# Kernel optimization log

Measured on AMD Instinct MI355X. Metric: run time of the kernel, lower is better.

## Reference

```python
import jax, jax.numpy as jnp
import numpy as np

# Clos factorization for in=out=4096, middle_switch_multiplier=4:
BIN, B1, B2, B3, BOUT = 64, 64, 256, 64, 64
B, C, D = 2, 4096, 4096


def setup_inputs() -> dict:
    key = jax.random.key(0)
    ks = jax.random.split(key, 7)
    k = 1.0 / np.sqrt(D)
    x = jax.random.normal(ks[0], (B, C, D), dtype=jnp.float32)
    # kaiming_uniform(a=sqrt(5)) on [bin,b1,b2]-like tensors ~ uniform(-bound, bound)
    w1 = jax.random.uniform(ks[1], (BIN, B1, B2), jnp.float32, -k, k)
    w2 = jax.random.uniform(ks[2], (B1, B2, B3), jnp.float32, -k, k)
    w3 = jax.random.uniform(ks[3], (B2, B3, BOUT), jnp.float32, -k, k)
    bias1 = jax.random.uniform(ks[4], (B1,), jnp.float32, -k, k)
    bias2 = jax.random.uniform(ks[5], (B2,), jnp.float32, -k, k)
    bias3 = jax.random.uniform(ks[6], (B3,), jnp.float32, -k, k)
    return {"x": x, "w1": w1, "w2": w2, "w3": w3,
            "bias1": bias1, "bias2": bias2, "bias3": bias3}


def reference(x, w1, w2, w3, bias1, bias2, bias3):
    b, c, _ = x.shape
    h = x.reshape(b, c, BIN, B1)                      # [b,c,n=bin,r=b1]
    h = jnp.einsum('bcnr,nrm->bcmr', h, w1) + bias1   # [b,c,b2,b1] + bias over b1
    h = jnp.einsum('bcmr,rmn->bcnm', h, w2) + bias2   # [b,c,b3,b2] + bias over b2
    h = jnp.einsum('bcnm,mro->bcor', h, w3) + bias3   # [b,c,bout,b3] + bias over b3
    return h.reshape(b, c, -1)                        # [b,c,out_features]
```

## Files before the change

kernel.cpp:

```cpp
#include <hip/hip_runtime.h>
#include <stdint.h>
#include <stddef.h>

typedef __bf16 bf16_t;
typedef __bf16 bf16x8 __attribute__((ext_vector_type(8)));
typedef __bf16 bf16x4 __attribute__((ext_vector_type(4)));
typedef float f32x4 __attribute__((ext_vector_type(4)));

#define VMW(n) asm volatile("s_waitcnt vmcnt(" #n ")" ::: "memory")
#define CFENCE asm volatile("" ::: "memory")
#define RAWBAR              \
  do {                      \
    __builtin_amdgcn_s_barrier(); \
    CFENCE;                 \
  } while (0)

__device__ __forceinline__ void gload_lds16(const void* g, void* l) {
  __builtin_amdgcn_global_load_lds(
      (const __attribute__((address_space(1))) uint32_t*)g,
      (__attribute__((address_space(3))) uint32_t*)l, 16, 0, 0);
}

__global__ __launch_bounds__(256) void w2s_k(const float* __restrict__ w2,
                                             float* __restrict__ w2s) {
  const int r = blockIdx.x, m = threadIdx.x;
  const float4* p = (const float4*)(w2 + ((size_t)(r * 256 + m)) * 64);
  float s = 0.f;
#pragma unroll
  for (int i = 0; i < 16; ++i) {
    float4 v = p[i];
    s += (v.x + v.y) + (v.z + v.w);
  }
  w2s[r * 256 + m] = s;
}

__global__ __launch_bounds__(256) void prep_k(
    const float* __restrict__ w1, const float* __restrict__ w3,
    const float* __restrict__ w2s, const float* __restrict__ bias1,
    const float* __restrict__ bias2, bf16_t* __restrict__ w1t,
    bf16_t* __restrict__ w3pt, float* __restrict__ c2) {
  __shared__ float lds[64][65];
  const int b = blockIdx.x;
  const int t = threadIdx.x;
  if (b == 512) {
    float s = 64.f * bias2[t];
#pragma unroll 8
    for (int r = 0; r < 64; ++r) s += bias1[r] * w2s[r * 256 + t];
    c2[t] = s;
    return;
  }
  if (b < 256) {
    const int k0 = (b >> 2) * 64;
    const int mt = (b & 3) * 64;
#pragma unroll
    for (int it = 0; it < 16; ++it) {
      int idx = t + it * 256;
      int kl = idx >> 6, ml = idx & 63;
      int k = k0 + kl;
      lds[kl][ml] = w1[(size_t)k * 256 + mt + ml] * w2s[(k & 63) * 256 + mt + ml];
    }
    __syncthreads();
#pragma unroll
    for (int it = 0; it < 16; ++it) {
      int idx = t + it * 256;
      int ml = idx >> 6, kl = idx & 63;
      w1t[(size_t)(mt + ml) * 4096 + k0 + kl] = (bf16_t)lds[kl][ml];
    }
    return;
  }
  const int b2 = b - 256;
  const int r = b2 & 63;
  const int mt = (b2 >> 6) * 64;
#pragma unroll
  for (int it = 0; it < 16; ++it) {
    int idx = t + it * 256;
    int ml = idx >> 6, o = idx & 63;
    lds[ml][o] = w3[(size_t)(mt + ml) * 4096 + r * 64 + o];
  }
  __syncthreads();
#pragma unroll
  for (int it = 0; it < 16; ++it) {
    int idx = t + it * 256;
    int o = idx >> 6, ml = idx & 63;
    w3pt[(size_t)(o * 64 + r) * 256 + mt + ml] = (bf16_t)lds[ml][o];
  }
}

__global__ __launch_bounds__(256, 2) void gemm1_k(
    const float* __restrict__ X, const bf16_t* __restrict__ W1T,
    bf16_t* __restrict__ S4) {
  __shared__ __align__(16) bf16_t lA[2][64 * 64];
  __shared__ __align__(16) bf16_t lB[2][256 * 64];
  const int tid = threadIdx.x;
  const int lane = tid & 63;
  const int wv = tid >> 6;
  const int bid = (int)blockIdx.x;
  const int xcd = bid & 7;
  const int rest = bid >> 3;
  const int mtile = xcd * 16 + (rest >> 2);
  const int ks = rest & 3;
  const size_t m0 = (size_t)mtile * 64;
  const int kbase = ks * 1024;
  const int wm = wv >> 1, wn = wv & 1;
  const int ar = tid >> 2;
  const int acg = tid & 3;

  f32x4 acc[2][8];
#pragma unroll
  for (int i = 0; i < 2; ++i)
#pragma unroll
    for (int j = 0; j < 8; ++j) acc[i][j] = (f32x4){0.f, 0.f, 0.f, 0.f};

  float4 aR[4];

  auto issueA = [&](int kt) {
#pragma unroll
    for (int j = 0; j < 4; ++j) {
      int f4 = acg + j * 4;
      aR[j] = *(const float4*)(X + (m0 + ar) * 4096 + (size_t)(kbase + kt * 64 + f4 * 4));
    }
  };
  auto writeA = [&](int buf) {
#pragma unroll
    for (int j = 0; j < 4; ++j) {
      int f4 = acg + j * 4;
      int off = ar * 128 + ((f4 * 8) ^ ((ar & 7) << 4));
      bf16x4 v;
      v[0] = (bf16_t)aR[j].x;
      v[1] = (bf16_t)aR[j].y;
      v[2] = (bf16_t)aR[j].z;
      v[3] = (bf16_t)aR[j].w;
      *(bf16x4*)((char*)(&lA[buf][0]) + off) = v;
    }
  };
  auto issueB = [&](int buf, int kt) {
#pragma unroll
    for (int i = 0; i < 8; ++i) {
      int row = wv * 64 + i * 8 + (lane >> 3);
      int srckb = ((lane & 7) * 16) ^ ((row & 7) << 4);
      const char* src = (const char*)W1T + (size_t)row * 8192 + (size_t)(kbase + kt * 64) * 2 + srckb;
      char* dst = (char*)(&lB[buf][0]) + (wv * 64 + i * 8) * 128;
      gload_lds16(src, dst);
    }
  };
  auto compute = [&](int buf) {
#pragma unroll
    for (int kk = 0; kk < 2; ++kk) {
      const int kb = kk * 64 + ((lane >> 4) * 16);
      bf16x8 af[2], bfr[8];
#pragma unroll
      for (int mf = 0; mf < 2; ++mf) {
        int row = wm * 32 + mf * 16 + (lane & 15);
        int off = row * 128 + (kb ^ ((row & 7) << 4));
        af[mf] = *(const bf16x8*)((const char*)(&lA[buf][0]) + off);
      }
#pragma unroll
      for (int nf = 0; nf < 8; ++nf) {
        int row = wn * 128 + nf * 16 + (lane & 15);
        int off = row * 128 + (kb ^ ((row & 7) << 4));
        bfr[nf] = *(const bf16x8*)((const char*)(&lB[buf][0]) + off);
      }
#pragma unroll
      for (int mf = 0; mf < 2; ++mf)
#pragma unroll
        for (int nf = 0; nf < 8; ++nf)
          acc[mf][nf] = __builtin_amdgcn_mfma_f32_16x16x32_bf16(af[mf], bfr[nf], acc[mf][nf], 0, 0, 0);
    }
  };

  issueA(0);
  issueB(0, 0);
  writeA(0);
  __syncthreads();

#pragma unroll 1
  for (int kt = 0; kt < 16; ++kt) {
    int cur = kt & 1;
    bool more = (kt + 1) < 16;
    if (more) {
      issueA(kt + 1);
      issueB(cur ^ 1, kt + 1);
    }
    compute(cur);
    if (more) writeA(cur ^ 1);
    __syncthreads();
  }

#pragma unroll
  for (int nf = 0; nf < 8; ++nf) {
    int col = wn * 128 + nf * 16 + (lane & 15);
#pragma unroll
    for (int mf = 0; mf < 2; ++mf) {
#pragma unroll
      for (int q = 0; q < 4; ++q) {
        int row = wm * 32 + mf * 16 + (lane >> 4) * 4 + q;
        S4[(m0 + row) * 1024 + (size_t)(ks * 256 + col)] = (bf16_t)acc[mf][nf][q];
      }
    }
  }
}

__global__ __launch_bounds__(256) void reduce_k(
    const bf16_t* __restrict__ S4, const float* __restrict__ c2,
    bf16_t* __restrict__ S) {
  const int bid = (int)blockIdx.x;
  const int base = (bid & 7) * 1024 + (bid >> 3) * 8;
  const int t = threadIdx.x;
  const int row = base + (t >> 5);
  const int c8 = (t & 31) << 3;
  float s[8];
  float4 ca = *(const float4*)(c2 + c8);
  float4 cb = *(const float4*)(c2 + c8 + 4);
  s[0] = ca.x; s[1] = ca.y; s[2] = ca.z; s[3] = ca.w;
  s[4] = cb.x; s[5] = cb.y; s[6] = cb.z; s[7] = cb.w;
#pragma unroll
  for (int h = 0; h < 4; ++h) {
    bf16x8 v = *(const bf16x8*)(S4 + (size_t)row * 1024 + h * 256 + c8);
#pragma unroll
    for (int j = 0; j < 8; ++j) s[j] += (float)v[j];
  }
  bf16x8 o;
#pragma unroll
  for (int j = 0; j < 8; ++j) o[j] = (bf16_t)s[j];
  *(bf16x8*)(S + (size_t)row * 256 + c8) = o;
}

__global__ __launch_bounds__(512, 2) void gemm2_k(
    const bf16_t* __restrict__ S, const bf16_t* __restrict__ W3pT,
    const float* __restrict__ bias3, float* __restrict__ OUT) {
  __shared__ __align__(16) bf16_t lA[2][128 * 64];
  __shared__ __align__(16) bf16_t lB[2][256 * 64];
  const int tid = threadIdx.x;
  const int lane = tid & 63;
  const int wv = tid >> 6;
  const int bid = (int)blockIdx.x;
  const int xcd = bid & 7;
  const int rest = bid >> 3;
  const int mt = xcd * 8 + (rest >> 4);
  const int nt = rest & 15;
  const size_t m0 = (size_t)mt * 128;
  const int n0 = nt * 256;
  const int wm = wv >> 2, wn = wv & 3;

  f32x4 acc[4][4];
#pragma unroll
  for (int i = 0; i < 4; ++i)
#pragma unroll
    for (int j = 0; j < 4; ++j) acc[i][j] = (f32x4){0.f, 0.f, 0.f, 0.f};

  auto stage = [&](int buf, int kt) {
#pragma unroll
    for (int i = 0; i < 2; ++i) {
      int row = wv * 16 + i * 8 + (lane >> 3);
      int srckb = ((lane & 7) * 16) ^ ((row & 7) << 4);
      const char* srcA = (const char*)S + (m0 + row) * 512 + (size_t)(kt * 128) + srckb;
      char* dstA = (char*)(&lA[buf][0]) + (wv * 16 + i * 8) * 128;
      gload_lds16(srcA, dstA);
    }
#pragma unroll
    for (int i = 0; i < 4; ++i) {
      int row = wv * 32 + i * 8 + (lane >> 3);
      int srckb = ((lane & 7) * 16) ^ ((row & 7) << 4);
      const char* srcB = (const char*)W3pT + (size_t)(n0 + row) * 512 + (size_t)(kt * 128) + srckb;
      char* dstB = (char*)(&lB[buf][0]) + (wv * 32 + i * 8) * 128;
      gload_lds16(srcB, dstB);
    }
  };
  auto compute = [&](int buf) {
#pragma unroll
    for (int kk = 0; kk < 2; ++kk) {
      const int kb = kk * 64 + ((lane >> 4) * 16);
      bf16x8 af[4], bfr[4];
#pragma unroll
      for (int mf = 0; mf < 4; ++mf) {
        int row = wm * 64 + mf * 16 + (lane & 15);
        int off = row * 128 + (kb ^ ((row & 7) << 4));
        af[mf] = *(const bf16x8*)((const char*)(&lA[buf][0]) + off);
      }
#pragma unroll
      for (int nf = 0; nf < 4; ++nf) {
        int row = wn * 64 + nf * 16 + (lane & 15);
        int off = row * 128 + (kb ^ ((row & 7) << 4));
        bfr[nf] = *(const bf16x8*)((const char*)(&lB[buf][0]) + off);
      }
#pragma unroll
      for (int mf = 0; mf < 4; ++mf)
#pragma unroll
        for (int nf = 0; nf < 4; ++nf)
          acc[mf][nf] = __builtin_amdgcn_mfma_f32_16x16x32_bf16(af[mf], bfr[nf], acc[mf][nf], 0, 0, 0);
    }
  };

  stage(0, 0);
  CFENCE;
  stage(1, 1);
  CFENCE;
  VMW(6);
  RAWBAR;
  compute(0);
  RAWBAR;
  stage(0, 2);
  CFENCE;
  VMW(6);
  RAWBAR;
  compute(1);
  RAWBAR;
  stage(1, 3);
  CFENCE;
  VMW(6);
  RAWBAR;
  compute(0);
  RAWBAR;
  VMW(0);
  RAWBAR;
  compute(1);

#pragma unroll
  for (int nf = 0; nf < 4; ++nf) {
    int jcol = wn * 64 + nf * 16 + (lane & 15);
    float b3 = bias3[jcol & 63];
    int j = n0 + jcol;
#pragma unroll
    for (int mf = 0; mf < 4; ++mf) {
#pragma unroll
      for (int q = 0; q < 4; ++q) {
        size_t row = m0 + (size_t)(wm * 64 + mf * 16 + (lane >> 4) * 4 + q);
        OUT[row * 4096 + j] = acc[mf][nf][q] + b3;
      }
    }
  }
}

extern "C" void kernel_launch(void* const* d_in, const int* in_sizes, int n_in,
                              void* d_out, int out_size, void* d_ws, size_t ws_size,
                              hipStream_t stream) {
  (void)in_sizes; (void)n_in; (void)out_size; (void)ws_size;
  const float* x  = (const float*)d_in[0];
  const float* w1 = (const float*)d_in[1];
  const float* w2 = (const float*)d_in[2];
  const float* w3 = (const float*)d_in[3];
  const float* b1 = (const float*)d_in[4];
  const float* b2 = (const float*)d_in[5];
  const float* b3 = (const float*)d_in[6];
  float* out = (float*)d_out;
  char* ws = (char*)d_ws;

  float*  w2s  = (float*)(ws + 0);
  float*  c2   = (float*)(ws + 65536);
  bf16_t* w1t  = (bf16_t*)(ws + 69632);
  bf16_t* w3pt = (bf16_t*)(ws + 69632 + 2097152);
  bf16_t* S4   = (bf16_t*)(ws + 69632 + 2 * 2097152);
  bf16_t* S    = (bf16_t*)(ws + 69632 + 2 * 2097152 + 16777216);

  w2s_k<<<64, 256, 0, stream>>>(w2, w2s);
  prep_k<<<513, 256, 0, stream>>>(w1, w3, w2s, b1, b2, w1t, w3pt, c2);
  gemm1_k<<<512, 256, 0, stream>>>(x, w1t, S4);
  reduce_k<<<1024, 256, 0, stream>>>(S4, c2, S);
  gemm2_k<<<1024, 512, 0, stream>>>(S, w3pt, b3, out);
}
```

Baseline: 104.5 us.

## Restructure gemm1 to LDS-free per-wave tiles with 8-way split-K

gemm1 now gives each wave its own 32x256 output tile over a 512-wide K slice, loading X and W1T fragments straight from global into registers for the MFMAs. The double-buffered LDS staging and the block-level barriers are removed. The split-K factor goes from 4 to 8, which doubles the S4 partial-sum buffer, and reduce_k sums 8 partials. The result tile is staged through per-wave LDS so S4 gets coalesced 16-byte stores. The trade-off is losing LDS reuse of B across waves and doubling partial-sum traffic, in exchange for no synchronisation and more independent waves.

```diff
diff --git a/kernel.cpp b/kernel.cpp
--- a/kernel.cpp
+++ b/kernel.cpp
@@ -8,6 +8,7 @@
 typedef float f32x4 __attribute__((ext_vector_type(4)));
 
 #define VMW(n) asm volatile("s_waitcnt vmcnt(" #n ")" ::: "memory")
+#define LGKM0 asm volatile("s_waitcnt lgkmcnt(0)" ::: "memory")
 #define CFENCE asm volatile("" ::: "memory")
 #define RAWBAR              \
   do {                      \
@@ -89,133 +90,94 @@
 __global__ __launch_bounds__(256, 2) void gemm1_k(
     const float* __restrict__ X, const bf16_t* __restrict__ W1T,
     bf16_t* __restrict__ S4) {
-  __shared__ __align__(16) bf16_t lA[2][64 * 64];
-  __shared__ __align__(16) bf16_t lB[2][256 * 64];
+  __shared__ __align__(16) bf16_t eps[4][32 * 256];
   const int tid = threadIdx.x;
   const int lane = tid & 63;
   const int wv = tid >> 6;
-  const int bid = (int)blockIdx.x;
-  const int xcd = bid & 7;
-  const int rest = bid >> 3;
-  const int mtile = xcd * 16 + (rest >> 2);
-  const int ks = rest & 3;
-  const size_t m0 = (size_t)mtile * 64;
-  const int kbase = ks * 1024;
-  const int wm = wv >> 1, wn = wv & 1;
-  const int ar = tid >> 2;
-  const int acg = tid & 3;
-
-  f32x4 acc[2][8];
+  const int w = (int)blockIdx.x * 4 + wv;
+  const int rowgrp = w >> 3;
+  const int ks = w & 7;
+  const size_t m0 = (size_t)rowgrp * 32;
+  const int kbase = ks * 512;
+  const int lr = lane & 15;
+  const int lk = (lane >> 4) * 8;
+
+  f32x4 acc[2][16];
 #pragma unroll
   for (int i = 0; i < 2; ++i)
 #pragma unroll
-    for (int j = 0; j < 8; ++j) acc[i][j] = (f32x4){0.f, 0.f, 0.f, 0.f};
-
-  float4 aR[4];
-
-  auto issueA = [&](int kt) {
-#pragma unroll
-    for (int j = 0; j < 4; ++j) {
-      int f4 = acg + j * 4;
-      aR[j] = *(const float4*)(X + (m0 + ar) * 4096 + (size_t)(kbase + kt * 64 + f4 * 4));
-    }
-  };
-  auto writeA = [&](int buf) {
-#pragma unroll
-    for (int j = 0; j < 4; ++j) {
-      int f4 = acg + j * 4;
-      int off = ar * 128 + ((f4 * 8) ^ ((ar & 7) << 4));
-      bf16x4 v;
-      v[0] = (bf16_t)aR[j].x;
-      v[1] = (bf16_t)aR[j].y;
-      v[2] = (bf16_t)aR[j].z;
-      v[3] = (bf16_t)aR[j].w;
-      *(bf16x4*)((char*)(&lA[buf][0]) + off) = v;
-    }
-  };
-  auto issueB = [&](int buf, int kt) {
-#pragma unroll
-    for (int i = 0; i < 8; ++i) {
-      int row = wv * 64 + i * 8 + (lane >> 3);
-      int srckb = ((lane & 7) * 16) ^ ((row & 7) << 4);
-      const char* src = (const char*)W1T + (size_t)row * 8192 + (size_t)(kbase + kt * 64) * 2 + srckb;
-      char* dst = (char*)(&lB[buf][0]) + (wv * 64 + i * 8) * 128;
-      gload_lds16(src, dst);
-    }
-  };
-  auto compute = [&](int buf) {
-#pragma unroll
-    for (int kk = 0; kk < 2; ++kk) {
-      const int kb = kk * 64 + ((lane >> 4) * 16);
-      bf16x8 af[2], bfr[8];
-#pragma unroll
-      for (int mf = 0; mf < 2; ++mf) {
-        int row = wm * 32 + mf * 16 + (lane & 15);
-        int off = row * 128 + (kb ^ ((row & 7) << 4));
-        af[mf] = *(const bf16x8*)((const char*)(&lA[buf][0]) + off);
+    for (int j = 0; j < 16; ++j) acc[i][j] = (f32x4){0.f, 0.f, 0.f, 0.f};
+
+  const float* xb0 = X + (m0 + lr) * 4096 + (size_t)(kbase + lk);
+  const float* xb1 = X + (m0 + 16 + lr) * 4096 + (size_t)(kbase + lk);
+  const bf16_t* bb = W1T + (size_t)lr * 4096 + (size_t)(kbase + lk);
+
+#pragma unroll 2
+  for (int kt = 0; kt < 16; ++kt) {
+    const int ko = kt * 32;
+    float4 u0 = *(const float4*)(xb0 + ko);
+    float4 v0 = *(const float4*)(xb0 + ko + 4);
+    float4 u1 = *(const float4*)(xb1 + ko);
+    float4 v1 = *(const float4*)(xb1 + ko + 4);
+    bf16x8 a0, a1;
+    a0[0] = (bf16_t)u0.x; a0[1] = (bf16_t)u0.y; a0[2] = (bf16_t)u0.z; a0[3] = (bf16_t)u0.w;
+    a0[4] = (bf16_t)v0.x; a0[5] = (bf16_t)v0.y; a0[6] = (bf16_t)v0.z; a0[7] = (bf16_t)v0.w;
+    a1[0] = (bf16_t)u1.x; a1[1] = (bf16_t)u1.y; a1[2] = (bf16_t)u1.z; a1[3] = (bf16_t)u1.w;
+    a1[4] = (bf16_t)v1.x; a1[5] = (bf16_t)v1.y; a1[6] = (bf16_t)v1.z; a1[7] = (bf16_t)v1.w;
+#pragma unroll
+    for (int g = 0; g < 4; ++g) {
+      bf16x8 b0 = *(const bf16x8*)(bb + (size_t)(g * 4 + 0) * 16 * 4096 + ko);
+      bf16x8 b1 = *(const bf16x8*)(bb + (size_t)(g * 4 + 1) * 16 * 4096 + ko);
+      bf16x8 b2 = *(const bf16x8*)(bb + (size_t)(g * 4 + 2) * 16 * 4096 + ko);
+      bf16x8 b3 = *(const bf16x8*)(bb + (size_t)(g * 4 + 3) * 16 * 4096 + ko);
+      acc[0][g * 4 + 0] = __builtin_amdgcn_mfma_f32_16x16x32_bf16(a0, b0, acc[0][g * 4 + 0], 0, 0, 0);
+      acc[1][g * 4 + 0] = __builtin_amdgcn_mfma_f32_16x16x32_bf16(a1, b0, acc[1][g * 4 + 0], 0, 0, 0);
+      acc[0][g * 4 + 1] = __builtin_amdgcn_mfma_f32_16x16x32_bf16(a0, b1, acc[0][g * 4 + 1], 0, 0, 0);
+      acc[1][g * 4 + 1] = __builtin_amdgcn_mfma_f32_16x16x32_bf16(a1, b1, acc[1][g * 4 + 1], 0, 0, 0);
+      acc[0][g * 4 + 2] = __builtin_amdgcn_mfma_f32_16x16x32_bf16(a0, b2, acc[0][g * 4 + 2], 0, 0, 0);
+      acc[1][g * 4 + 2] = __builtin_amdgcn_mfma_f32_16x16x32_bf16(a1, b2, acc[1][g * 4 + 2], 0, 0, 0);
+      acc[0][g * 4 + 3] = __builtin_amdgcn_mfma_f32_16x16x32_bf16(a0, b3, acc[0][g * 4 + 3], 0, 0, 0);
+      acc[1][g * 4 + 3] = __builtin_amdgcn_mfma_f32_16x16x32_bf16(a1, b3, acc[1][g * 4 + 3], 0, 0, 0);
+    }
+  }
+
+  bf16_t* ep = &eps[wv][0];
+#pragma unroll
+  for (int mf = 0; mf < 2; ++mf)
+#pragma unroll
+    for (int nf = 0; nf < 16; ++nf)
+#pragma unroll
+      for (int q = 0; q < 4; ++q) {
+        int row = mf * 16 + (lane >> 4) * 4 + q;
+        int col = nf * 16 + lr;
+        ep[row * 256 + col] = (bf16_t)acc[mf][nf][q];
       }
-#pragma unroll
-      for (int nf = 0; nf < 8; ++nf) {
-        int row = wn * 128 + nf * 16 + (lane & 15);
-        int off = row * 128 + (kb ^ ((row & 7) << 4));
-        bfr[nf] = *(const bf16x8*)((const char*)(&lB[buf][0]) + off);
-      }
-#pragma unroll
-      for (int mf = 0; mf < 2; ++mf)
-#pragma unroll
-        for (int nf = 0; nf < 8; ++nf)
-          acc[mf][nf] = __builtin_amdgcn_mfma_f32_16x16x32_bf16(af[mf], bfr[nf], acc[mf][nf], 0, 0, 0);
-    }
-  };
-
-  issueA(0);
-  issueB(0, 0);
-  writeA(0);
-  __syncthreads();
-
-#pragma unroll 1
-  for (int kt = 0; kt < 16; ++kt) {
-    int cur = kt & 1;
-    bool more = (kt + 1) < 16;
-    if (more) {
-      issueA(kt + 1);
-      issueB(cur ^ 1, kt + 1);
-    }
-    compute(cur);
-    if (more) writeA(cur ^ 1);
-    __syncthreads();
-  }
-
-#pragma unroll
-  for (int nf = 0; nf < 8; ++nf) {
-    int col = wn * 128 + nf * 16 + (lane & 15);
-#pragma unroll
-    for (int mf = 0; mf < 2; ++mf) {
-#pragma unroll
-      for (int q = 0; q < 4; ++q) {
-        int row = wm * 32 + mf * 16 + (lane >> 4) * 4 + q;
-        S4[(m0 + row) * 1024 + (size_t)(ks * 256 + col)] = (bf16_t)acc[mf][nf][q];
-      }
-    }
+  LGKM0;
+  __builtin_amdgcn_sched_barrier(0);
+#pragma unroll
+  for (int it = 0; it < 16; ++it) {
+    int chunk = it * 64 + lane;
+    int row = chunk >> 5;
+    int c8 = (chunk & 31) << 3;
+    bf16x8 v = *(const bf16x8*)(ep + row * 256 + c8);
+    *(bf16x8*)(S4 + (m0 + row) * 2048 + (size_t)(ks * 256 + c8)) = v;
   }
 }
 
 __global__ __launch_bounds__(256) void reduce_k(
     const bf16_t* __restrict__ S4, const float* __restrict__ c2,
     bf16_t* __restrict__ S) {
-  const int bid = (int)blockIdx.x;
-  const int base = (bid & 7) * 1024 + (bid >> 3) * 8;
-  const int t = threadIdx.x;
-  const int row = base + (t >> 5);
-  const int c8 = (t & 31) << 3;
+  const int gid = (int)blockIdx.x * 256 + threadIdx.x;
+  const int row = gid >> 5;
+  const int c8 = (gid & 31) << 3;
   float s[8];
   float4 ca = *(const float4*)(c2 + c8);
   float4 cb = *(const float4*)(c2 + c8 + 4);
   s[0] = ca.x; s[1] = ca.y; s[2] = ca.z; s[3] = ca.w;
   s[4] = cb.x; s[5] = cb.y; s[6] = cb.z; s[7] = cb.w;
 #pragma unroll
-  for (int h = 0; h < 4; ++h) {
-    bf16x8 v = *(const bf16x8*)(S4 + (size_t)row * 1024 + h * 256 + c8);
+  for (int h = 0; h < 8; ++h) {
+    bf16x8 v = *(const bf16x8*)(S4 + (size_t)row * 2048 + h * 256 + c8);
 #pragma unroll
     for (int j = 0; j < 8; ++j) s[j] += (float)v[j];
   }
@@ -349,8 +311,8 @@
   float*  c2   = (float*)(ws + 65536);
   bf16_t* w1t  = (bf16_t*)(ws + 69632);
   bf16_t* w3pt = (bf16_t*)(ws + 69632 + 2097152);
-  bf16_t* S4   = (bf16_t*)(ws + 69632 + 2 * 2097152);
-  bf16_t* S    = (bf16_t*)(ws + 69632 + 2 * 2097152 + 16777216);
+  bf16_t* S4   = (bf16_t*)(ws + 69632 + 4194304);
+  bf16_t* S    = (bf16_t*)(ws + 69632 + 4194304 + 33554432);
 
   w2s_k<<<64, 256, 0, stream>>>(w2, w2s);
   prep_k<<<513, 256, 0, stream>>>(w1, w3, w2s, b1, b2, w1t, w3pt, c2);
```

After: 147.7 us. 1.41x slower.
